# Performance work log

Hardware: AMD Instinct MI355X
Metric: run time of the kernel (lower is better)

Reference implementation:

```python
import jax, jax.numpy as jnp
import numpy as np

B = 4; IMG = 32; P = 2; C_IN = 3; H_DIM = 384; DEPTH = 8
GS = IMG // P; L = GS * GS
NSTATE = 16; KDIR = 4; DIN = 384; RANK = 24; MH = int(H_DIM * 4.0)
BOT = 128; NCLS = 1000; TFREQ = 256


def _silu(x):
    return x * jax.nn.sigmoid(x)


def _rms(x, w, eps=1e-6):
    return x * jax.lax.rsqrt(jnp.mean(x * x, -1, keepdims=True) + eps) * w


def _ln(x, w, b, eps=1e-5):
    mu = jnp.mean(x, -1, keepdims=True)
    v = jnp.mean((x - mu) ** 2, -1, keepdims=True)
    return (x - mu) * jax.lax.rsqrt(v + eps) * w + b


def _ln_na(x, eps=1e-6):
    mu = jnp.mean(x, -1, keepdims=True)
    v = jnp.mean((x - mu) ** 2, -1, keepdims=True)
    return (x - mu) * jax.lax.rsqrt(v + eps)


def _mod(x, shift, scale):
    return x * (1.0 + scale[:, None, :]) + shift[:, None, :]


def _ss2d(xin, in_w, conv_w, conv_b, xproj_w, dt_w, dt_b, A_logs, Ds, onorm_w, onorm_b, outp_w):
    Bb = xin.shape[0]
    z = xin @ in_w.T  # (B,L,DIN)
    z2d = z.reshape(Bb, GS, GS, DIN).transpose(0, 3, 1, 2)  # (B,DIN,H,W)
    z2d = jax.lax.conv_general_dilated(z2d, conv_w, (1, 1), 'SAME',
        feature_group_count=DIN, dimension_numbers=('NCHW', 'OIHW', 'NCHW'))
    z2d = _silu(z2d + conv_b[None, :, None, None])
    # cross_scan -> (B,K,DIN,L): row-major, reversed, col-major, reversed col-major
    s1 = z2d.reshape(Bb, DIN, L)
    s3 = z2d.transpose(0, 1, 3, 2).reshape(Bb, DIN, L)
    xs = jnp.stack([s1, s1[..., ::-1], s3, s3[..., ::-1]], axis=1)
    x_dbl = jnp.einsum('bkdl,kod->bkol', xs, xproj_w)
    dtr = x_dbl[:, :, :RANK]
    Bssm = x_dbl[:, :, RANK:RANK + NSTATE]   # (B,K,N,L)
    Cssm = x_dbl[:, :, RANK + NSTATE:]       # (B,K,N,L)
    dt = jnp.einsum('bkrl,kdr->bkdl', dtr, dt_w)
    dt = jax.nn.softplus(dt + dt_b[None, :, :, None])
    A = -jnp.exp(A_logs)                     # (K,DIN,N)
    dA = jnp.exp(jnp.einsum('bkdl,kdn->bkldn', dt, A))
    dBu = jnp.einsum('bkdl,bknl->bkldn', dt * xs, Bssm)
    def comb(e1, e2):
        a1, b1 = e1
        a2, b2 = e2
        return a1 * a2, a2 * b1 + b2
    _, hs = jax.lax.associative_scan(comb, (dA, dBu), axis=2)  # h over token axis
    ys = jnp.einsum('bkldn,bknl->bkdl', hs, Cssm) + Ds[None, :, :, None] * xs
    # cross_merge: undo each direction's reorder and sum
    m1 = ys[:, 0]
    m2 = ys[:, 1][..., ::-1]
    m3 = ys[:, 2].reshape(Bb, DIN, GS, GS).swapaxes(2, 3).reshape(Bb, DIN, L)
    m4 = ys[:, 3][..., ::-1].reshape(Bb, DIN, GS, GS).swapaxes(2, 3).reshape(Bb, DIN, L)
    out = (m1 + m2 + m3 + m4).transpose(0, 2, 1)  # (B,L,DIN)
    out = _ln(out, onorm_w, onorm_b)
    return out @ outp_w.T


def _forward(x, t, y, t_w1, t_b1, t_w2, t_b2, y_table, pe_w1, pe_w2, pe_b2, pos_embed,
             adaln_w, adaln_b, n1_w, n2_w, in_w, conv_w, conv_b, xproj_w, dt_w, dt_b,
             A_logs, Ds, onorm_w, onorm_b, outp_w, mlp_w1, mlp_b1, mlp_w2, mlp_b2,
             f_adaln_w, f_adaln_b, f_lin_w, f_lin_b):
    # timestep embedding (DiT TimestepEmbedder, freq dim 256)
    half = TFREQ // 2
    freqs = jnp.exp(-jnp.log(10000.0) * jnp.arange(half, dtype=jnp.float32) / half)
    ang = t[:, None] * freqs[None]
    temb = jnp.concatenate([jnp.cos(ang), jnp.sin(ang)], axis=-1)
    temb = _silu(temb @ t_w1.T + t_b1) @ t_w2.T + t_b2
    c = temb + y_table[y]  # (B,H_DIM)
    # bottleneck patch embed: patchify -> bottleneck linear -> hidden linear
    xp = x.reshape(B, C_IN, GS, P, GS, P).transpose(0, 2, 4, 1, 3, 5).reshape(B, L, C_IN * P * P)
    h = (xp @ pe_w1.T) @ pe_w2.T + pe_b2
    h = h + pos_embed
    for i in range(DEPTH):
        mod = _silu(c) @ adaln_w[i].T + adaln_b[i]
        sh1, sc1, g1, sh2, sc2, g2 = jnp.split(mod, 6, axis=-1)
        h = h + g1[:, None] * _ss2d(_mod(_rms(h, n1_w[i]), sh1, sc1),
            in_w[i], conv_w[i], conv_b[i], xproj_w[i], dt_w[i], dt_b[i],
            A_logs[i], Ds[i], onorm_w[i], onorm_b[i], outp_w[i])
        u = _mod(_rms(h, n2_w[i]), sh2, sc2)
        u12 = u @ mlp_w1[i].T + mlp_b1[i]
        u1, u2 = jnp.split(u12, 2, axis=-1)
        h = h + g2[:, None] * ((_silu(u1) * u2) @ mlp_w2[i].T + mlp_b2[i])
    modf = _silu(c) @ f_adaln_w.T + f_adaln_b
    shf, scf = jnp.split(modf, 2, axis=-1)
    h = _mod(_ln_na(h), shf, scf)
    out = h @ f_lin_w.T + f_lin_b  # (B,L,P*P*C_IN)
    out = out.reshape(B, GS, GS, P, P, C_IN)
    out = jnp.einsum('nhwpqc->nchpwq', out)
    return out.reshape(B, C_IN, IMG, IMG)


def _sincos_1d(dim, pos):
    omega = 1.0 / (10000.0 ** (np.arange(dim // 2, dtype=np.float64) / (dim / 2.0)))
    out = pos.reshape(-1)[:, None] * omega[None, :]
    return np.concatenate([np.sin(out), np.cos(out)], axis=1)


def _pos_embed_np(dim, gs):
    g = np.stack(np.meshgrid(np.arange(gs, dtype=np.float64), np.arange(gs, dtype=np.float64)), axis=0)
    return np.concatenate([_sincos_1d(dim // 2, g[0]), _sincos_1d(dim // 2, g[1])], axis=1).astype(np.float32)


def setup_inputs():
    key = jax.random.key(0)
    ks = iter(jax.random.split(key, 64))
    nrm = lambda shape, s=0.02: jax.random.normal(next(ks), shape, jnp.float32) * s
    d = {}
    d['x'] = jax.random.normal(next(ks), (B, C_IN, IMG, IMG), jnp.float32)
    d['t'] = jax.random.uniform(next(ks), (B,), jnp.float32) * 1000.0
    d['y'] = jax.random.randint(next(ks), (B,), 0, NCLS)
    d['t_w1'] = nrm((H_DIM, TFREQ)); d['t_b1'] = jnp.zeros((H_DIM,), jnp.float32)
    d['t_w2'] = nrm((H_DIM, H_DIM)); d['t_b2'] = jnp.zeros((H_DIM,), jnp.float32)
    d['y_table'] = nrm((NCLS, H_DIM))
    d['pe_w1'] = nrm((BOT, C_IN * P * P), 0.1)
    d['pe_w2'] = nrm((H_DIM, BOT), 0.1); d['pe_b2'] = jnp.zeros((H_DIM,), jnp.float32)
    d['pos_embed'] = jnp.asarray(_pos_embed_np(H_DIM, GS))[None]
    d['adaln_w'] = nrm((DEPTH, 6 * H_DIM, H_DIM)); d['adaln_b'] = jnp.zeros((DEPTH, 6 * H_DIM), jnp.float32)
    d['n1_w'] = jnp.ones((DEPTH, H_DIM), jnp.float32); d['n2_w'] = jnp.ones((DEPTH, H_DIM), jnp.float32)
    d['in_w'] = nrm((DEPTH, DIN, H_DIM), 0.05)
    d['conv_w'] = nrm((DEPTH, DIN, 1, 3, 3), 0.1); d['conv_b'] = jnp.zeros((DEPTH, DIN), jnp.float32)
    d['xproj_w'] = nrm((DEPTH, KDIR, RANK + 2 * NSTATE, DIN), 0.05)
    d['dt_w'] = nrm((DEPTH, KDIR, DIN, RANK), 0.1)
    d['dt_b'] = nrm((DEPTH, KDIR, DIN), 0.5)
    d['A_logs'] = jnp.tile(jnp.log(jnp.arange(1, NSTATE + 1, dtype=jnp.float32))[None, None, None, :], (DEPTH, KDIR, DIN, 1))
    d['Ds'] = jnp.ones((DEPTH, KDIR, DIN), jnp.float32)
    d['onorm_w'] = jnp.ones((DEPTH, DIN), jnp.float32); d['onorm_b'] = jnp.zeros((DEPTH, DIN), jnp.float32)
    d['outp_w'] = nrm((DEPTH, H_DIM, DIN), 0.05)
    d['mlp_w1'] = nrm((DEPTH, 2 * MH, H_DIM)); d['mlp_b1'] = jnp.zeros((DEPTH, 2 * MH), jnp.float32)
    d['mlp_w2'] = nrm((DEPTH, H_DIM, MH)); d['mlp_b2'] = jnp.zeros((DEPTH, H_DIM), jnp.float32)
    d['f_adaln_w'] = nrm((2 * H_DIM, H_DIM)); d['f_adaln_b'] = jnp.zeros((2 * H_DIM,), jnp.float32)
    d['f_lin_w'] = nrm((P * P * C_IN, H_DIM)); d['f_lin_b'] = jnp.zeros((P * P * C_IN,), jnp.float32)
    return d


def reference(x, t, y, t_w1, t_b1, t_w2, t_b2, y_table, pe_w1, pe_w2, pe_b2, pos_embed,
              adaln_w, adaln_b, n1_w, n2_w, in_w, conv_w, conv_b, xproj_w, dt_w, dt_b,
              A_logs, Ds, onorm_w, onorm_b, outp_w, mlp_w1, mlp_b1, mlp_w2, mlp_b2,
              f_adaln_w, f_adaln_b, f_lin_w, f_lin_b):
    return _forward(x, t, y, t_w1, t_b1, t_w2, t_b2, y_table, pe_w1, pe_w2, pe_b2, pos_embed,
                    adaln_w, adaln_b, n1_w, n2_w, in_w, conv_w, conv_b, xproj_w, dt_w, dt_b,
                    A_logs, Ds, onorm_w, onorm_b, outp_w, mlp_w1, mlp_b1, mlp_w2, mlp_b2,
                    f_adaln_w, f_adaln_b, f_lin_w, f_lin_b)
```

## Files before the change

### kernel.cpp

```cpp
#include <hip/hip_runtime.h>
#include <hip/hip_bf16.h>
#include <math.h>


#define DEV __device__ __forceinline__

typedef __bf16 bf16_t;
typedef __attribute__((ext_vector_type(8))) __bf16 bf16x8;
typedef __attribute__((ext_vector_type(4))) float f32x4;
typedef __attribute__((ext_vector_type(2))) _Float16 h2;

DEV float siluf(float x){ return x / (1.f + __expf(-x)); }
DEV float softplusf(float x){ return fmaxf(x, 0.f) + __logf(1.f + __expf(-fabsf(x))); }

DEV int perm_idx(int k, int l){
  switch(k & 3){
    case 0: return l;
    case 1: return 255 - l;
    case 2: return ((l & 15) << 4) | (l >> 4);
    default: { int r = 255 - l; return ((r & 15) << 4) | (r >> 4); }
  }
}

DEV void cvt_one(int idx, const float* inw, const float* outw, const float* w1,
                 const float* w2, const float* xp, bf16_t* dst){
  const float* src; int off;
  if (idx < 147456){ src = inw;  off = idx; }
  else if (idx < 294912){ src = outw; off = idx - 147456; }
  else if (idx < 1474560){
    int o = idx - 294912;
    int rowc = o / 384, col = o - rowc*384;
    int q = rowc >> 5, tt = rowc & 31;
    int srow = (tt < 16) ? (q*16 + tt) : (1536 + q*16 + (tt - 16));
    src = w1; off = srow*384 + col;
  }
  else if (idx < 2064384){ src = w2; off = idx - 1474560; }
  else { src = xp; off = idx - 2064384; }
  float4 v = *(const float4*)(src + off);
  union { bf16_t h[4]; uint2 u; } cv;
  cv.h[0] = (bf16_t)v.x; cv.h[1] = (bf16_t)v.y; cv.h[2] = (bf16_t)v.z; cv.h[3] = (bf16_t)v.w;
  *(uint2*)(dst + idx) = cv.u;
}

__global__ void k_cvt_layer(const float* __restrict__ inw, const float* __restrict__ outw,
                            const float* __restrict__ w1, const float* __restrict__ w2,
                            const float* __restrict__ xp, bf16_t* __restrict__ dst){
  int idx = (blockIdx.x*256 + threadIdx.x)*4;
  cvt_one(idx, inw, outw, w1, w2, xp, dst);
}

__global__ void k_cvt_all(const float* __restrict__ inw, const float* __restrict__ outw,
                          const float* __restrict__ w1, const float* __restrict__ w2,
                          const float* __restrict__ xp, bf16_t* __restrict__ dst){
  int layer = blockIdx.x / 2100;
  int within = blockIdx.x % 2100;
  int idx = (within*256 + threadIdx.x)*4;
  cvt_one(idx, inw + (size_t)layer*147456, outw + (size_t)layer*147456,
          w1 + (size_t)layer*1179648, w2 + (size_t)layer*589824,
          xp + (size_t)layer*86016, dst + (size_t)layer*2150400);
}

__global__ void k_cond1(const float* __restrict__ t, const float* __restrict__ tw1,
                        const float* __restrict__ tb1, float* __restrict__ h1g){
  int b = blockIdx.x / 3, ch = blockIdx.x % 3;
  int tid = threadIdx.x;
  int o = ch*128 + tid;
  __shared__ float temb[256];
  float tv = t[b];
  {
    float f = __expf(-logf(10000.f) * (float)tid / 128.f);
    float a = tv * f;
    temb[tid] = cosf(a); temb[128 + tid] = sinf(a);
  }
  __syncthreads();
  const float4* te = (const float4*)temb;
  const float4* wp = (const float4*)(tw1 + (size_t)o*256);
  float acc = tb1[o];
  #pragma unroll 8
  for (int j = 0; j < 64; j++){
    float4 c4 = te[j], w4 = wp[j];
    acc += c4.x*w4.x + c4.y*w4.y + c4.z*w4.z + c4.w*w4.w;
  }
  h1g[b*384 + o] = siluf(acc);
}

__global__ void k_cond2(const int* __restrict__ y, const float* __restrict__ h1g,
                        const float* __restrict__ tw2, const float* __restrict__ tb2,
                        const float* __restrict__ ytab, float* __restrict__ sc){
  int b = blockIdx.x / 3, ch = blockIdx.x % 3;
  int tid = threadIdx.x;
  int o = ch*128 + tid;
  __shared__ float h1[384];
  h1[tid] = h1g[b*384 + tid];
  h1[tid + 128] = h1g[b*384 + tid + 128];
  h1[tid + 256] = h1g[b*384 + tid + 256];
  __syncthreads();
  const float4* hp = (const float4*)h1;
  const float4* wp = (const float4*)(tw2 + (size_t)o*384);
  float acc = tb2[o];
  #pragma unroll 8
  for (int j = 0; j < 96; j++){
    float4 c4 = hp[j], w4 = wp[j];
    acc += c4.x*w4.x + c4.y*w4.y + c4.z*w4.z + c4.w*w4.w;
  }
  float c = acc + ytab[(size_t)y[b]*384 + o];
  sc[b*384 + o] = siluf(c);
}

__global__ void k_patch(const float* __restrict__ x, const float* __restrict__ pw1,
                        const float* __restrict__ pw2, const float* __restrict__ pb2,
                        const float* __restrict__ pos, float* __restrict__ h){
  int bl = blockIdx.x; int b = bl >> 8; int l = bl & 255;
  int gh = l >> 4, gw = l & 15;
  __shared__ float xp[12]; __shared__ float tmp[128];
  int tid = threadIdx.x;
  if (tid < 12){
    int ci = tid >> 2, ph = (tid >> 1) & 1, pw = tid & 1;
    xp[tid] = x[((size_t)(b*3 + ci)*32 + gh*2 + ph)*32 + gw*2 + pw];
  }
  __syncthreads();
  if (tid < 128){
    float a = 0.f;
    #pragma unroll
    for (int k = 0; k < 12; k++) a += xp[k] * pw1[tid*12 + k];
    tmp[tid] = a;
  }
  __syncthreads();
  float a = pb2[tid];
  for (int j = 0; j < 128; j++) a += tmp[j] * pw2[(size_t)tid*128 + j];
  h[(size_t)(b*256 + l)*384 + tid] = a + pos[(size_t)l*384 + tid];
}

__global__ void k_lin_small(const float* __restrict__ sc, const float* __restrict__ W,
                            const float* __restrict__ bias, float* __restrict__ out, int N){
  int idx = blockIdx.x * blockDim.x + threadIdx.x;
  if (idx >= 4*N) return;
  int b = idx / N, o = idx % N;
  const float4* cp = (const float4*)(sc + b*384);
  const float4* wp = (const float4*)(W + (size_t)o*384);
  float a = bias[o];
  #pragma unroll 4
  for (int k = 0; k < 96; k++){
    float4 c4 = cp[k], w4 = wp[k];
    a += c4.x*w4.x + c4.y*w4.y + c4.z*w4.z + c4.w*w4.w;
  }
  out[idx] = a;
}

__global__ void k_rms_mod(const float* __restrict__ h, const float* __restrict__ nw,
                          const float* __restrict__ modBase, bf16_t* __restrict__ out){
  int bl = blockIdx.x; int b = bl >> 8;
  const float* hp = h + (size_t)bl*384;
  const float* mp = modBase + (size_t)b*18432;
  __shared__ float red[2];
  int tid = threadIdx.x;
  float v[3]; float ss = 0.f;
  #pragma unroll
  for (int ii = 0; ii < 3; ii++){ v[ii] = hp[tid + ii*128]; ss += v[ii]*v[ii]; }
  #pragma unroll
  for (int off = 32; off; off >>= 1) ss += __shfl_down(ss, off);
  if ((tid & 63) == 0) red[tid >> 6] = ss;
  __syncthreads();
  ss = red[0] + red[1];
  float inv = rsqrtf(ss / 384.f + 1e-6f);
  #pragma unroll
  for (int ii = 0; ii < 3; ii++){
    int d = tid + ii*128;
    float xv = v[ii] * inv * nw[d];
    out[(size_t)bl*384 + d] = (bf16_t)(xv * (1.f + mp[384 + d]) + mp[d]);
  }
}

template<int MODE>
__global__ __launch_bounds__(256) void k_gemm_bf(
    const bf16_t* __restrict__ A, const bf16_t* __restrict__ W,
    const float* __restrict__ bias, float* __restrict__ C,
    const float* __restrict__ modBase, int N, int K, int Nstore){
  __shared__ bf16_t As[2][64*40];
  __shared__ bf16_t Ws[2][64*40];
  const int tid = threadIdx.x;
  const int bm = blockIdx.y * 64, bn = blockIdx.x * 64;
  const int wave = tid >> 6, lane = tid & 63;
  const int m16 = lane & 15, kg = lane >> 4;
  const int r = tid >> 2, seg = tid & 3;
  const int nt = K / 32;

  uint4 aP, wP;
  auto loadT = [&](int kt){
    wP = *(const uint4*)(W + (size_t)(bn + r)*K + kt*32 + seg*8);
    aP = *(const uint4*)(A + (size_t)(bm + r)*K + kt*32 + seg*8);
  };
  auto stash = [&](int buf){
    *(uint4*)&As[buf][r*40 + seg*8] = aP;
    *(uint4*)&Ws[buf][r*40 + seg*8] = wP;
  };

  f32x4 acc[4] = {};
  loadT(0); stash(0); __syncthreads();
  for (int kt = 0; kt < nt; kt++){
    int buf = kt & 1;
    if (kt + 1 < nt) loadT(kt + 1);
    bf16x8 af = *(bf16x8*)&As[buf][(wave*16 + m16)*40 + kg*8];
    #pragma unroll
    for (int j = 0; j < 4; j++){
      bf16x8 bfr = *(bf16x8*)&Ws[buf][(j*16 + m16)*40 + kg*8];
      acc[j] = __builtin_amdgcn_mfma_f32_16x16x32_bf16(af, bfr, acc[j], 0, 0, 0);
    }
    if (kt + 1 < nt) stash(buf ^ 1);
    __syncthreads();
  }

  if constexpr (MODE == 4){
    bf16_t* Cb = (bf16_t*)C;
    const int Np = N >> 1;
    #pragma unroll
    for (int jp = 0; jp < 2; jp++){
      int pcol = (bn >> 1) + jp*16 + m16;
      float b1v = bias[pcol], b2v = bias[Np + pcol];
      #pragma unroll
      for (int rg = 0; rg < 4; rg++){
        int row = bm + wave*16 + kg*4 + rg;
        float u1v = acc[jp*2][rg] + b1v;
        float u2v = acc[jp*2 + 1][rg] + b2v;
        Cb[(size_t)row*Np + pcol] = (bf16_t)(siluf(u1v)*u2v);
      }
    }
  } else {
    #pragma unroll
    for (int j = 0; j < 4; j++){
      int col = bn + j*16 + m16;
      if (col < Nstore){
        #pragma unroll
        for (int rg = 0; rg < 4; rg++){
          int row = bm + wave*16 + kg*4 + rg;
          float v = acc[j][rg];
          if constexpr (MODE == 5) v += bias[col];
          if constexpr (MODE == 2 || MODE == 5)
            C[(size_t)row*N + col] += modBase[(size_t)(row >> 8)*18432 + col] * v;
          else
            C[(size_t)row*N + col] = v;
        }
      }
    }
  }
}

__global__ void k_conv(const float* __restrict__ z, const float* __restrict__ cw,
                       const float* __restrict__ cb, float* __restrict__ convT,
                       bf16_t* __restrict__ convB){
  int bl = blockIdx.x; int b = bl >> 8, l = bl & 255;
  int hh = l >> 4, ww = l & 15;
  int d = threadIdx.x;
  float acc = cb[d];
  #pragma unroll
  for (int kh = 0; kh < 3; kh++){
    int yy = hh + kh - 1; if ((unsigned)yy > 15u) continue;
    #pragma unroll
    for (int kw = 0; kw < 3; kw++){
      int xx = ww + kw - 1; if ((unsigned)xx > 15u) continue;
      acc += z[(size_t)(b*256 + yy*16 + xx)*384 + d] * cw[d*9 + kh*3 + kw];
    }
  }
  float s = siluf(acc);
  convT[(size_t)bl*384 + d] = s;
  convB[(size_t)bl*384 + d] = (bf16_t)s;
}

__global__ __launch_bounds__(256) void k_scan(
    const float* __restrict__ xdblS, const float* __restrict__ convT,
    const float* __restrict__ dtw, const float* __restrict__ dtb,
    const float* __restrict__ Alog, const float* __restrict__ Dsw,
    float* __restrict__ ysT){
  int blk = blockIdx.x;
  int dp = blk % 192; int k = (blk / 192) & 3; int b = blk / 768;
  int d0 = dp*2;
  int tid = threadIdx.x;
  int n = tid & 15, chunk = tid >> 4;
  __shared__ float sdt[2][256], sxv[2][256], sy[2][256];
  __shared__ float sA[2][16][17], sBc[2][16][17], sPre[2][16][17];
  __shared__ _Float16 sB16[256*18];
  __shared__ _Float16 sC16[256*18];

  {
    int l = tid;
    int lp = perm_idx(k, l);
    const float* row = xdblS + (size_t)(b*256 + lp)*224 + k*56;
    const float4* xr = (const float4*)(row);
    float4 x0 = xr[0], x1 = xr[1], x2 = xr[2], x3 = xr[3], x4 = xr[4], x5 = xr[5];
    #pragma unroll
    for (int j = 0; j < 2; j++){
      const float4* w = (const float4*)(dtw + ((size_t)k*384 + d0 + j)*24);
      float4 w0 = w[0], w1 = w[1], w2 = w[2], w3 = w[3], w4 = w[4], w5 = w[5];
      float a0 = dtb[k*384 + d0 + j];
      a0 += x0.x*w0.x + x0.y*w0.y + x0.z*w0.z + x0.w*w0.w;
      a0 += x1.x*w1.x + x1.y*w1.y + x1.z*w1.z + x1.w*w1.w;
      a0 += x2.x*w2.x + x2.y*w2.y + x2.z*w2.z + x2.w*w2.w;
      a0 += x3.x*w3.x + x3.y*w3.y + x3.z*w3.z + x3.w*w3.w;
      a0 += x4.x*w4.x + x4.y*w4.y + x4.z*w4.z + x4.w*w4.w;
      a0 += x5.x*w5.x + x5.y*w5.y + x5.z*w5.z + x5.w*w5.w;
      sdt[j][l] = softplusf(a0);
    }
    float2 xv2 = *(const float2*)(convT + (size_t)(b*256 + lp)*384 + d0);
    sxv[0][l] = xv2.x; sxv[1][l] = xv2.y;
    const float4* bp = (const float4*)(row + 24);
    h2* bl = (h2*)(sB16 + l*18);
    h2* cl = (h2*)(sC16 + l*18);
    #pragma unroll
    for (int q = 0; q < 4; q++){
      float4 bv = bp[q];
      h2 p0; p0[0] = (_Float16)bv.x; p0[1] = (_Float16)bv.y;
      h2 p1; p1[0] = (_Float16)bv.z; p1[1] = (_Float16)bv.w;
      bl[q*2] = p0; bl[q*2+1] = p1;
      float4 cv = bp[q+4];
      h2 q0; q0[0] = (_Float16)cv.x; q0[1] = (_Float16)cv.y;
      h2 q1; q1[0] = (_Float16)cv.z; q1[1] = (_Float16)cv.w;
      cl[q*2] = q0; cl[q*2+1] = q1;
    }
  }
  __syncthreads();

  float av[2], Dv[2];
  #pragma unroll
  for (int j = 0; j < 2; j++){
    av[j] = -__expf(Alog[((size_t)(k*384) + d0 + j)*16 + n]);
    Dv[j] = Dsw[k*384 + d0 + j];
  }

  float dA[2][16], dBu[2][16];
  float Ap[2] = {1.f, 1.f}, hl[2] = {0.f, 0.f};
  #pragma unroll
  for (int i = 0; i < 16; i++){
    int l = chunk*16 + i;
    float bn16 = (float)sB16[l*18 + n];
    #pragma unroll
    for (int j = 0; j < 2; j++){
      float dtv = sdt[j][l];
      float e = __expf(dtv * av[j]);
      float u = dtv * sxv[j][l] * bn16;
      dA[j][i] = e; dBu[j][i] = u;
      Ap[j] *= e; hl[j] = e*hl[j] + u;
    }
  }
  #pragma unroll
  for (int j = 0; j < 2; j++){ sA[j][chunk][n] = Ap[j]; sBc[j][chunk][n] = hl[j]; }
  __syncthreads();

  if (tid < 32){
    int j = tid >> 4, nn = tid & 15;
    float carry = 0.f;
    #pragma unroll
    for (int c = 0; c < 16; c++){
      sPre[j][c][nn] = carry;
      carry = sA[j][c][nn]*carry + sBc[j][c][nn];
    }
  }
  __syncthreads();

  float hh[2] = {sPre[0][chunk][n], sPre[1][chunk][n]};
  #pragma unroll
  for (int i = 0; i < 16; i++){
    int l = chunk*16 + i;
    float cn = (float)sC16[l*18 + n];
    hh[0] = dA[0][i]*hh[0] + dBu[0][i];
    hh[1] = dA[1][i]*hh[1] + dBu[1][i];
    float p0 = hh[0]*cn, p1 = hh[1]*cn;
    p0 += __shfl_xor(p0, 1); p1 += __shfl_xor(p1, 1);
    p0 += __shfl_xor(p0, 2); p1 += __shfl_xor(p1, 2);
    p0 += __shfl_xor(p0, 4); p1 += __shfl_xor(p1, 4);
    p0 += __shfl_xor(p0, 8); p1 += __shfl_xor(p1, 8);
    if (n == 0){
      sy[0][l] = p0 + Dv[0]*sxv[0][l];
      sy[1][l] = p1 + Dv[1]*sxv[1][l];
    }
  }
  __syncthreads();
  ysT[((size_t)(b*4 + k)*384 + d0)*256 + tid] = sy[0][tid];
  ysT[((size_t)(b*4 + k)*384 + d0 + 1)*256 + tid] = sy[1][tid];
}

__global__ void k_merge_ln(const float* __restrict__ ysT, const float* __restrict__ ow,
                           const float* __restrict__ ob, bf16_t* __restrict__ out){
  int bl = blockIdx.x; int b = bl >> 8; int l = bl & 255;
  int tl = ((l & 15) << 4) | (l >> 4);
  int i2 = 255 - l, i4 = 255 - tl;
  __shared__ float red[4];
  int tid = threadIdx.x;
  const float* base = ysT + (size_t)b*4*384*256;
  float v[3]; float s = 0.f, s2 = 0.f;
  #pragma unroll
  for (int ii = 0; ii < 3; ii++){
    int d = tid + ii*128;
    float vv = base[(size_t)d*256 + l]
             + base[(size_t)(384 + d)*256 + i2]
             + base[(size_t)(768 + d)*256 + tl]
             + base[(size_t)(1152 + d)*256 + i4];
    v[ii] = vv; s += vv; s2 += vv*vv;
  }
  #pragma unroll
  for (int off = 32; off; off >>= 1){ s += __shfl_down(s, off); s2 += __shfl_down(s2, off); }
  if ((tid & 63) == 0){ red[tid >> 6] = s; red[2 + (tid >> 6)] = s2; }
  __syncthreads();
  s = red[0] + red[1]; s2 = red[2] + red[3];
  float mu = s / 384.f;
  float var = s2 / 384.f - mu*mu;
  float inv = rsqrtf(var + 1e-5f);
  #pragma unroll
  for (int ii = 0; ii < 3; ii++){
    int d = tid + ii*128;
    out[(size_t)bl*384 + d] = (bf16_t)((v[ii] - mu) * inv * ow[d] + ob[d]);
  }
}

__global__ void k_final(const float* __restrict__ h, const float* __restrict__ modf,
                        const float* __restrict__ flw, const float* __restrict__ flb,
                        float* __restrict__ out){
  int bl = blockIdx.x; int b = bl >> 8; int l = bl & 255;
  int tid = threadIdx.x;
  __shared__ float buf[384]; __shared__ float red[4];
  const float* hp = h + (size_t)bl*384;
  float v[3]; float s = 0.f, s2 = 0.f;
  #pragma unroll
  for (int ii = 0; ii < 3; ii++){ float xv = hp[tid + ii*128]; v[ii] = xv; s += xv; s2 += xv*xv; }
  #pragma unroll
  for (int off = 32; off; off >>= 1){ s += __shfl_down(s, off); s2 += __shfl_down(s2, off); }
  if ((tid & 63) == 0){ red[tid >> 6] = s; red[2 + (tid >> 6)] = s2; }
  __syncthreads();
  s = red[0] + red[1]; s2 = red[2] + red[3];
  float mu = s / 384.f;
  float var = s2 / 384.f - mu*mu;
  float inv = rsqrtf(var + 1e-6f);
  #pragma unroll
  for (int ii = 0; ii < 3; ii++){
    int d = tid + ii*128;
    buf[d] = (v[ii] - mu) * inv * (1.f + modf[b*768 + 384 + d]) + modf[b*768 + d];
  }
  __syncthreads();
  if (tid < 12){
    float a = flb[tid];
    for (int k = 0; k < 384; k++) a += buf[k] * flw[(size_t)tid*384 + k];
    int p = tid / 6, q = (tid / 3) & 1, cc = tid % 3;
    int gh = l >> 4, gw = l & 15;
    out[((size_t)(b*3 + cc)*32 + gh*2 + p)*32 + gw*2 + q] = a;
  }
}

extern "C" void kernel_launch(void* const* d_in, const int* in_sizes, int n_in,
                              void* d_out, int out_size, void* d_ws, size_t ws_size,
                              hipStream_t stream){
  const float* x       = (const float*)d_in[0];
  const float* t       = (const float*)d_in[1];
  const int*   y       = (const int*)  d_in[2];
  const float* t_w1    = (const float*)d_in[3];
  const float* t_b1    = (const float*)d_in[4];
  const float* t_w2    = (const float*)d_in[5];
  const float* t_b2    = (const float*)d_in[6];
  const float* y_table = (const float*)d_in[7];
  const float* pe_w1   = (const float*)d_in[8];
  const float* pe_w2   = (const float*)d_in[9];
  const float* pe_b2   = (const float*)d_in[10];
  const float* pos     = (const float*)d_in[11];
  const float* adaln_w = (const float*)d_in[12];
  const float* adaln_b = (const float*)d_in[13];
  const float* n1_w    = (const float*)d_in[14];
  const float* n2_w    = (const float*)d_in[15];
  const float* in_w    = (const float*)d_in[16];
  const float* conv_w  = (const float*)d_in[17];
  const float* conv_b  = (const float*)d_in[18];
  const float* xproj_w = (const float*)d_in[19];
  const float* dt_w    = (const float*)d_in[20];
  const float* dt_b    = (const float*)d_in[21];
  const float* A_logs  = (const float*)d_in[22];
  const float* Ds      = (const float*)d_in[23];
  const float* onorm_w = (const float*)d_in[24];
  const float* onorm_b = (const float*)d_in[25];
  const float* outp_w  = (const float*)d_in[26];
  const float* mlp_w1  = (const float*)d_in[27];
  const float* mlp_b1  = (const float*)d_in[28];
  const float* mlp_w2  = (const float*)d_in[29];
  const float* mlp_b2  = (const float*)d_in[30];
  const float* f_adaln_w = (const float*)d_in[31];
  const float* f_adaln_b = (const float*)d_in[32];
  const float* f_lin_w = (const float*)d_in[33];
  const float* f_lin_b = (const float*)d_in[34];

  float* ws = (float*)d_ws;
  float*  sc      = ws + 0;
  float*  h       = ws + 1536;
  float*  modAll  = ws + 394752;
  float*  modf    = ws + 468480;
  float*  buf1    = ws + 471552;
  float*  convT   = ws + 864768;
  float*  xdblS   = ws + 1257984;
  bf16_t* u12b    = (bf16_t*)(ws + 1487360);
  float*  ysT     = ws + 2273792;
  bf16_t* xin_bf  = (bf16_t*)(ws + 3846656);
  bf16_t* ssin_bf = (bf16_t*)(ws + 4043264);
  bf16_t* conv_bf = (bf16_t*)(ws + 4239872);
  bf16_t* wbfBase = (bf16_t*)(ws + 4436480);
  float*  h1g     = ysT;

  const bool bigws = ws_size >= (size_t)13038080 * 4;

  k_cond1<<<dim3(12), dim3(128), 0, stream>>>(t, t_w1, t_b1, h1g);
  k_cond2<<<dim3(12), dim3(128), 0, stream>>>(y, h1g, t_w2, t_b2, y_table, sc);
  k_patch<<<dim3(1024), dim3(384), 0, stream>>>(x, pe_w1, pe_w2, pe_b2, pos, h);
  k_lin_small<<<dim3(288), dim3(256), 0, stream>>>(sc, adaln_w, adaln_b, modAll, 18432);
  if (bigws)
    k_cvt_all<<<dim3(16800), dim3(256), 0, stream>>>(
        in_w, outp_w, mlp_w1, mlp_w2, xproj_w, wbfBase);

  for (int i = 0; i < 8; i++){
    const float* modL = modAll + (size_t)i*2304;
    bf16_t* wbf = bigws ? wbfBase + (size_t)i*2150400 : wbfBase;
    if (!bigws)
      k_cvt_layer<<<dim3(2100), dim3(256), 0, stream>>>(
          in_w + (size_t)i*147456, outp_w + (size_t)i*147456, mlp_w1 + (size_t)i*1179648,
          mlp_w2 + (size_t)i*589824, xproj_w + (size_t)i*86016, wbf);
    bf16_t* wbf_in  = wbf;
    bf16_t* wbf_out = wbf + 147456;
    bf16_t* wbf_w1  = wbf + 294912;
    bf16_t* wbf_w2  = wbf + 1474560;
    bf16_t* wbf_xp  = wbf + 2064384;

    k_rms_mod<<<dim3(1024), dim3(128), 0, stream>>>(h, n1_w + i*384, modL + 0, xin_bf);
    k_gemm_bf<0><<<dim3(6,16), dim3(256), 0, stream>>>(
        xin_bf, wbf_in, nullptr, buf1, nullptr, 384, 384, 384);
    k_conv<<<dim3(1024), dim3(384), 0, stream>>>(
        buf1, conv_w + (size_t)i*384*9, conv_b + i*384, convT, conv_bf);
    k_gemm_bf<0><<<dim3(4,16), dim3(256), 0, stream>>>(
        conv_bf, wbf_xp, nullptr, xdblS, nullptr, 224, 384, 224);
    k_scan<<<dim3(3072), dim3(256), 0, stream>>>(
        xdblS, convT, dt_w + (size_t)i*4*384*24, dt_b + (size_t)i*4*384,
        A_logs + (size_t)i*4*384*16, Ds + (size_t)i*4*384, ysT);
    k_merge_ln<<<dim3(1024), dim3(128), 0, stream>>>(
        ysT, onorm_w + i*384, onorm_b + i*384, ssin_bf);
    k_gemm_bf<2><<<dim3(6,16), dim3(256), 0, stream>>>(
        ssin_bf, wbf_out, nullptr, h, modL + 768, 384, 384, 384);
    k_rms_mod<<<dim3(1024), dim3(128), 0, stream>>>(h, n2_w + i*384, modL + 1152, xin_bf);
    k_gemm_bf<4><<<dim3(48,16), dim3(256), 0, stream>>>(
        xin_bf, wbf_w1, mlp_b1 + (size_t)i*3072, (float*)u12b, nullptr, 3072, 384, 3072);
    k_gemm_bf<5><<<dim3(6,16), dim3(256), 0, stream>>>(
        u12b, wbf_w2, mlp_b2 + (size_t)i*384, h, modL + 1920, 384, 1536, 384);
  }

  k_lin_small<<<dim3(12), dim3(256), 0, stream>>>(sc, f_adaln_w, f_adaln_b, modf, 768);
  k_final<<<dim3(1024), dim3(128), 0, stream>>>(h, modf, f_lin_w, f_lin_b, (float*)d_out);
}
```

Measured before the change: 1.159 ms.

## Fuse first RMSNorm+modulation into in-proj GEMM and store scan output token-major

The first k_rms_mod launch per layer is removed. The in-projection GEMM now reads the fp32 hidden state directly, computes each row's RMS in a prologue, and applies the norm, scale and shift while packing bf16 A tiles. Separately, the scan writes its outputs in a (token, channel) layout so that k_merge_ln reads contiguous rows instead of strided columns. This saves one launch and an intermediate round trip per layer. In exchange, every column block recomputes the row norms and reads more fp32 data, and the scan's stores become narrow strided float2 writes.

```diff
diff --git a/kernel.cpp b/kernel.cpp
--- a/kernel.cpp
+++ b/kernel.cpp
@@ -171,11 +171,12 @@
   }
 }
 
-template<int MODE>
+template<int MODE, int ASRC>
 __global__ __launch_bounds__(256) void k_gemm_bf(
-    const bf16_t* __restrict__ A, const bf16_t* __restrict__ W,
+    const void* __restrict__ Avoid, const bf16_t* __restrict__ W,
     const float* __restrict__ bias, float* __restrict__ C,
-    const float* __restrict__ modBase, int N, int K, int Nstore){
+    const float* __restrict__ modBase, const float* __restrict__ nw,
+    const float* __restrict__ modRms, int N, int K, int Nstore){
   __shared__ bf16_t As[2][64*40];
   __shared__ bf16_t Ws[2][64*40];
   const int tid = threadIdx.x;
@@ -185,10 +186,45 @@
   const int r = tid >> 2, seg = tid & 3;
   const int nt = K / 32;
 
+  float inv = 0.f;
+  if constexpr (ASRC == 2){
+    const float* hp = (const float*)Avoid + (size_t)(bm + r)*K + seg*8;
+    float ss = 0.f;
+    for (int kt = 0; kt < nt; kt++){
+      float4 a4 = *(const float4*)(hp + kt*32);
+      float4 b4 = *(const float4*)(hp + kt*32 + 4);
+      ss += a4.x*a4.x + a4.y*a4.y + a4.z*a4.z + a4.w*a4.w
+          + b4.x*b4.x + b4.y*b4.y + b4.z*b4.z + b4.w*b4.w;
+    }
+    ss += __shfl_xor(ss, 1);
+    ss += __shfl_xor(ss, 2);
+    inv = rsqrtf(ss / 384.f + 1e-6f);
+  }
+
   uint4 aP, wP;
   auto loadT = [&](int kt){
     wP = *(const uint4*)(W + (size_t)(bn + r)*K + kt*32 + seg*8);
-    aP = *(const uint4*)(A + (size_t)(bm + r)*K + kt*32 + seg*8);
+    if constexpr (ASRC == 2){
+      const float* Ap = (const float*)Avoid + (size_t)(bm + r)*K + kt*32 + seg*8;
+      float4 a4 = *(const float4*)(Ap), b4 = *(const float4*)(Ap + 4);
+      int d0 = kt*32 + seg*8;
+      const float* mp = modRms + (size_t)(bm >> 8)*18432;
+      float4 n0 = *(const float4*)(nw + d0),        n1 = *(const float4*)(nw + d0 + 4);
+      float4 sh0 = *(const float4*)(mp + d0),       sh1 = *(const float4*)(mp + d0 + 4);
+      float4 sc0 = *(const float4*)(mp + 384 + d0), sc1 = *(const float4*)(mp + 384 + d0 + 4);
+      union { bf16_t h[8]; uint4 u; } pk;
+      pk.h[0] = (bf16_t)((a4.x*inv*n0.x)*(1.f + sc0.x) + sh0.x);
+      pk.h[1] = (bf16_t)((a4.y*inv*n0.y)*(1.f + sc0.y) + sh0.y);
+      pk.h[2] = (bf16_t)((a4.z*inv*n0.z)*(1.f + sc0.z) + sh0.z);
+      pk.h[3] = (bf16_t)((a4.w*inv*n0.w)*(1.f + sc0.w) + sh0.w);
+      pk.h[4] = (bf16_t)((b4.x*inv*n1.x)*(1.f + sc1.x) + sh1.x);
+      pk.h[5] = (bf16_t)((b4.y*inv*n1.y)*(1.f + sc1.y) + sh1.y);
+      pk.h[6] = (bf16_t)((b4.z*inv*n1.z)*(1.f + sc1.z) + sh1.z);
+      pk.h[7] = (bf16_t)((b4.w*inv*n1.w)*(1.f + sc1.w) + sh1.w);
+      aP = pk.u;
+    } else {
+      aP = *(const uint4*)((const bf16_t*)Avoid + (size_t)(bm + r)*K + kt*32 + seg*8);
+    }
   };
   auto stash = [&](int buf){
     *(uint4*)&As[buf][r*40 + seg*8] = aP;
@@ -270,7 +306,7 @@
     const float* __restrict__ xdblS, const float* __restrict__ convT,
     const float* __restrict__ dtw, const float* __restrict__ dtb,
     const float* __restrict__ Alog, const float* __restrict__ Dsw,
-    float* __restrict__ ysT){
+    float* __restrict__ ysL){
   int blk = blockIdx.x;
   int dp = blk % 192; int k = (blk / 192) & 3; int b = blk / 768;
   int d0 = dp*2;
@@ -374,26 +410,27 @@
     }
   }
   __syncthreads();
-  ysT[((size_t)(b*4 + k)*384 + d0)*256 + tid] = sy[0][tid];
-  ysT[((size_t)(b*4 + k)*384 + d0 + 1)*256 + tid] = sy[1][tid];
-}
-
-__global__ void k_merge_ln(const float* __restrict__ ysT, const float* __restrict__ ow,
+  float2 o2; o2.x = sy[0][tid]; o2.y = sy[1][tid];
+  *(float2*)(ysL + ((size_t)(b*4 + k)*256 + tid)*384 + d0) = o2;
+}
+
+__global__ void k_merge_ln(const float* __restrict__ ysL, const float* __restrict__ ow,
                            const float* __restrict__ ob, bf16_t* __restrict__ out){
   int bl = blockIdx.x; int b = bl >> 8; int l = bl & 255;
   int tl = ((l & 15) << 4) | (l >> 4);
   int i2 = 255 - l, i4 = 255 - tl;
   __shared__ float red[4];
   int tid = threadIdx.x;
-  const float* base = ysT + (size_t)b*4*384*256;
+  const float* base = ysL + (size_t)b*4*256*384;
+  const float* r0 = base + ((size_t)(0*256 + l ))*384;
+  const float* r1 = base + ((size_t)(1*256 + i2))*384;
+  const float* r2 = base + ((size_t)(2*256 + tl))*384;
+  const float* r3 = base + ((size_t)(3*256 + i4))*384;
   float v[3]; float s = 0.f, s2 = 0.f;
   #pragma unroll
   for (int ii = 0; ii < 3; ii++){
     int d = tid + ii*128;
-    float vv = base[(size_t)d*256 + l]
-             + base[(size_t)(384 + d)*256 + i2]
-             + base[(size_t)(768 + d)*256 + tl]
-             + base[(size_t)(1152 + d)*256 + i4];
+    float vv = r0[d] + r1[d] + r2[d] + r3[d];
     v[ii] = vv; s += vv; s2 += vv*vv;
   }
   #pragma unroll
@@ -522,25 +559,25 @@
     bf16_t* wbf_w2  = wbf + 1474560;
     bf16_t* wbf_xp  = wbf + 2064384;
 
-    k_rms_mod<<<dim3(1024), dim3(128), 0, stream>>>(h, n1_w + i*384, modL + 0, xin_bf);
-    k_gemm_bf<0><<<dim3(6,16), dim3(256), 0, stream>>>(
-        xin_bf, wbf_in, nullptr, buf1, nullptr, 384, 384, 384);
+    k_gemm_bf<0,2><<<dim3(6,16), dim3(256), 0, stream>>>(
+        h, wbf_in, nullptr, buf1, nullptr, n1_w + i*384, modL + 0, 384, 384, 384);
     k_conv<<<dim3(1024), dim3(384), 0, stream>>>(
         buf1, conv_w + (size_t)i*384*9, conv_b + i*384, convT, conv_bf);
-    k_gemm_bf<0><<<dim3(4,16), dim3(256), 0, stream>>>(
-        conv_bf, wbf_xp, nullptr, xdblS, nullptr, 224, 384, 224);
+    k_gemm_bf<0,0><<<dim3(4,16), dim3(256), 0, stream>>>(
+        conv_bf, wbf_xp, nullptr, xdblS, nullptr, nullptr, nullptr, 224, 384, 224);
     k_scan<<<dim3(3072), dim3(256), 0, stream>>>(
         xdblS, convT, dt_w + (size_t)i*4*384*24, dt_b + (size_t)i*4*384,
         A_logs + (size_t)i*4*384*16, Ds + (size_t)i*4*384, ysT);
     k_merge_ln<<<dim3(1024), dim3(128), 0, stream>>>(
         ysT, onorm_w + i*384, onorm_b + i*384, ssin_bf);
-    k_gemm_bf<2><<<dim3(6,16), dim3(256), 0, stream>>>(
-        ssin_bf, wbf_out, nullptr, h, modL + 768, 384, 384, 384);
+    k_gemm_bf<2,0><<<dim3(6,16), dim3(256), 0, stream>>>(
+        ssin_bf, wbf_out, nullptr, h, modL + 768, nullptr, nullptr, 384, 384, 384);
     k_rms_mod<<<dim3(1024), dim3(128), 0, stream>>>(h, n2_w + i*384, modL + 1152, xin_bf);
-    k_gemm_bf<4><<<dim3(48,16), dim3(256), 0, stream>>>(
-        xin_bf, wbf_w1, mlp_b1 + (size_t)i*3072, (float*)u12b, nullptr, 3072, 384, 3072);
-    k_gemm_bf<5><<<dim3(6,16), dim3(256), 0, stream>>>(
-        u12b, wbf_w2, mlp_b2 + (size_t)i*384, h, modL + 1920, 384, 1536, 384);
+    k_gemm_bf<4,0><<<dim3(48,16), dim3(256), 0, stream>>>(
+        xin_bf, wbf_w1, mlp_b1 + (size_t)i*3072, (float*)u12b, nullptr, nullptr, nullptr,
+        3072, 384, 3072);
+    k_gemm_bf<5,0><<<dim3(6,16), dim3(256), 0, stream>>>(
+        u12b, wbf_w2, mlp_b2 + (size_t)i*384, h, modL + 1920, nullptr, nullptr, 384, 1536, 384);
   }
 
   k_lin_small<<<dim3(12), dim3(256), 0, stream>>>(sc, f_adaln_w, f_adaln_b, modf, 768);
```

Result: slower. 1.182 ms (+2.0%).
